# Performance work log

Measured on AMD Instinct MI355X. Metric: run time of the kernel, lower is better.

Reference implementation:

```python
import jax, jax.numpy as jnp
import numpy as np
from jax import lax

H = 64  # LSTM units (hard-coded in the module)


def _lstm(x, W, U, b, return_sequences):
    """Keras-style LSTM (inference; recurrent_dropout inactive).
    x: [B, T, F]; W: [F, 4H]; U: [H, 4H]; b: [4H].
    Gate order (Keras): i, f, g(cell), o.
    """
    B = x.shape[0]
    # Precompute input contribution for all timesteps: [T, B, 4H]
    xz = jnp.einsum('btf,fg->tbg', x, W) + b

    def step(carry, z_t):
        h, c = carry
        z = z_t + h @ U  # [B, 4H]
        i = jax.nn.sigmoid(z[:, :H])
        f = jax.nn.sigmoid(z[:, H:2 * H])
        g = jnp.tanh(z[:, 2 * H:3 * H])
        o = jax.nn.sigmoid(z[:, 3 * H:])
        c = f * c + i * g
        h = o * jnp.tanh(c)
        return (h, c), h

    init = (jnp.zeros((B, H), x.dtype), jnp.zeros((B, H), x.dtype))
    (h_last, _), hs = lax.scan(step, init, xz)
    if return_sequences:
        return jnp.transpose(hs, (1, 0, 2))  # [B, T, H]
    return h_last  # [B, H]


def setup_inputs() -> dict:
    key = jax.random.key(0)
    ks = jax.random.split(key, 8)
    B, T, F = 4096, 256, 32
    s_in = 1.0 / np.sqrt(F)
    s_h = 1.0 / np.sqrt(H)
    return {
        'x': jax.random.normal(ks[0], (B, T, F), jnp.float32),
        'W1': jax.random.normal(ks[1], (F, 4 * H), jnp.float32) * s_in,
        'U1': jax.random.normal(ks[2], (H, 4 * H), jnp.float32) * s_h,
        'b1': jnp.zeros((4 * H,), jnp.float32),
        'W2': jax.random.normal(ks[3], (H, 4 * H), jnp.float32) * s_h,
        'U2': jax.random.normal(ks[4], (H, 4 * H), jnp.float32) * s_h,
        'b2': jnp.zeros((4 * H,), jnp.float32),
        'Wd': jax.random.normal(ks[5], (H, H), jnp.float32) * s_h,
        'bd': jnp.zeros((H,), jnp.float32),
        'Wo': jax.random.normal(ks[6], (H, 1), jnp.float32) * s_h,
        'bo': jnp.zeros((1,), jnp.float32),
    }


def reference(x, W1, U1, b1, W2, U2, b2, Wd, bd, Wo, bo):
    h_seq = _lstm(x, W1, U1, b1, return_sequences=True)   # hidden_lstm
    h_last = _lstm(h_seq, W2, U2, b2, return_sequences=False)  # lstm_layer
    d = jax.nn.sigmoid(h_last @ Wd + bd)  # Dense(64, sigmoid)
    return jax.nn.sigmoid(d @ Wo + bo)    # Dense(1, sigmoid) -> [B, 1]
```

## Files before the change

kernel.cpp:

```cpp
#include <hip/hip_runtime.h>


typedef __attribute__((ext_vector_type(8))) short short8;
typedef __attribute__((ext_vector_type(4))) float floatx4;
typedef __attribute__((ext_vector_type(2))) float floatx2;

__device__ __forceinline__ float ex2(float x){ return __builtin_amdgcn_exp2f(x); }
__device__ __forceinline__ float rcp_(float x){ return __builtin_amdgcn_rcpf(x); }
__device__ __forceinline__ float sigm(float x){ return rcp_(1.0f + ex2(-1.44269504f*x)); }
__device__ __forceinline__ unsigned bfbits(float f){
    unsigned u = __builtin_bit_cast(unsigned, f);
    u += 0x7FFFu + ((u >> 16) & 1u);
    return u >> 16;
}
__device__ __forceinline__ short f2bf(float f){ return (short)bfbits(f); }
__device__ __forceinline__ unsigned pack_bf2(float a, float b){
    return bfbits(a) | (bfbits(b) << 16);
}

#define MFMA_BF16 __builtin_amdgcn_mfma_f32_16x16x32_bf16

__global__ __launch_bounds__(1024, 1)
void lstm2_tz(const float* __restrict__ x,
              const float* __restrict__ W1, const float* __restrict__ U1, const float* __restrict__ b1,
              const float* __restrict__ W2, const float* __restrict__ U2, const float* __restrict__ b2,
              const float* __restrict__ Wd, const float* __restrict__ bd,
              const float* __restrict__ Wo, const float* __restrict__ bo,
              float* __restrict__ out)
{
    __shared__ __align__(16) short h1b[2][16 * 72];
    __shared__ __align__(16) short h2b[2][16 * 72];
    __shared__ __align__(16) short xsb[2][16 * 40];
    __shared__ float psum[4][16];

    const int tid  = threadIdx.x;
    const int w    = tid >> 6;
    const bool isL1 = (w < 8);
    const int wv   = isL1 ? w : (w - 8);
    const int lane = tid & 63;
    const int n    = lane & 15;
    const int q    = lane >> 4;
    const int b0   = blockIdx.x * 16;

    const float LG = 1.44269504f;

    const int ugl = n >> 2;
    const int gA  = n & 3;
    const float sA = (gA == 2) ? (2.0f * LG) : (-LG);

    short8  Wa[8];
    floatx4 bC[2];
    if (isL1) {
#pragma unroll
        for (int tt = 0; tt < 2; ++tt) {
            const int t = wv * 2 + tt;
            const int ncol = gA * 64 + t * 4 + ugl;
#pragma unroll
            for (int j = 0; j < 8; ++j) {
                const int k = q * 8 + j;
                Wa[tt * 3 + 0][j] = f2bf(W1[k * 256 + ncol] * sA);
                Wa[tt * 3 + 1][j] = f2bf(U1[k * 256 + ncol] * sA);
                Wa[tt * 3 + 2][j] = f2bf(U1[(32 + k) * 256 + ncol] * sA);
            }
#pragma unroll
            for (int r = 0; r < 4; ++r)
                bC[tt][r] = b1[r * 64 + t * 4 + q] * ((r == 2) ? (2.0f * LG) : (-LG));
        }
    } else {
#pragma unroll
        for (int tt = 0; tt < 2; ++tt) {
            const int t = wv * 2 + tt;
            const int ncol = gA * 64 + t * 4 + ugl;
#pragma unroll
            for (int j = 0; j < 8; ++j) {
                const int k = q * 8 + j;
                Wa[tt * 4 + 0][j] = f2bf(W2[k * 256 + ncol] * sA);
                Wa[tt * 4 + 1][j] = f2bf(W2[(32 + k) * 256 + ncol] * sA);
                Wa[tt * 4 + 2][j] = f2bf(U2[k * 256 + ncol] * sA);
                Wa[tt * 4 + 3][j] = f2bf(U2[(32 + k) * 256 + ncol] * sA);
            }
#pragma unroll
            for (int r = 0; r < 4; ++r)
                bC[tt][r] = b2[r * 64 + t * 4 + q] * ((r == 2) ? (2.0f * LG) : (-LG));
        }
    }

    {
        unsigned* p1 = (unsigned*)&h1b[0][0];
        unsigned* p2 = (unsigned*)&h2b[0][0];
        for (int i = tid; i < 1152; i += 1024) { p1[i] = 0u; p2[i] = 0u; }
    }

    const int xr = tid >> 4;
    const int xc = (tid & 15) * 2;
    const float* xrow = x + (size_t)(b0 + xr) * 8192 + xc;
    floatx2 xv0;
    if (tid < 256) {
        floatx2 v = *(const floatx2*)xrow;
        *(unsigned*)&xsb[0][xr * 40 + xc] = pack_bf2(v.x, v.y);
        xv0 = *(const floatx2*)(xrow + 32);
    }
    __syncthreads();

    float c[2] = {0, 0};

    for (int u = 0; u <= 256; ++u) {
        const int par = u & 1, pax = par ^ 1;
        if (isL1) {
            if (u < 256) {
                short8 bx  = *(const short8*)&xsb[par][n * 40 + q * 8];
                short8 bh0 = *(const short8*)&h1b[pax][n * 72 + q * 8];
                short8 bh1 = *(const short8*)&h1b[pax][n * 72 + 32 + q * 8];
#pragma unroll
                for (int tt = 0; tt < 2; ++tt) {
                    floatx4 z = bC[tt];
                    z = MFMA_BF16(Wa[tt * 3 + 0], bx,  z, 0, 0, 0);
                    z = MFMA_BF16(Wa[tt * 3 + 1], bh0, z, 0, 0, 0);
                    z = MFMA_BF16(Wa[tt * 3 + 2], bh1, z, 0, 0, 0);
                    float iv = rcp_(1.0f + ex2(z[0]));
                    float fv = rcp_(1.0f + ex2(z[1]));
                    float rg = rcp_(1.0f + ex2(z[2]));
                    float ov = rcp_(1.0f + ex2(z[3]));
                    float gp = fmaf(-5.77078016f, rg, 2.88539008f);
                    c[tt] = fmaf(fv, c[tt], iv * gp);
                    float th = fmaf(-2.0f, rcp_(1.0f + ex2(c[tt])), 1.0f);
                    h1b[par][n * 72 + (wv * 2 + tt) * 4 + q] = f2bf(ov * th);
                }
                if (tid < 256 && u < 255) {
                    *(unsigned*)&xsb[pax][xr * 40 + xc] = pack_bf2(xv0.x, xv0.y);
                    if (u < 254) xv0 = *(const floatx2*)(xrow + (size_t)(u + 2) * 32);
                }
            }
        } else {
            if (u >= 1) {
                short8 bh0 = *(const short8*)&h1b[pax][n * 72 + q * 8];
                short8 bh1 = *(const short8*)&h1b[pax][n * 72 + 32 + q * 8];
                short8 bg0 = *(const short8*)&h2b[par][n * 72 + q * 8];
                short8 bg1 = *(const short8*)&h2b[par][n * 72 + 32 + q * 8];
#pragma unroll
                for (int tt = 0; tt < 2; ++tt) {
                    floatx4 z = bC[tt];
                    z = MFMA_BF16(Wa[tt * 4 + 0], bh0, z, 0, 0, 0);
                    z = MFMA_BF16(Wa[tt * 4 + 1], bh1, z, 0, 0, 0);
                    z = MFMA_BF16(Wa[tt * 4 + 2], bg0, z, 0, 0, 0);
                    z = MFMA_BF16(Wa[tt * 4 + 3], bg1, z, 0, 0, 0);
                    float iv = rcp_(1.0f + ex2(z[0]));
                    float fv = rcp_(1.0f + ex2(z[1]));
                    float rg = rcp_(1.0f + ex2(z[2]));
                    float ov = rcp_(1.0f + ex2(z[3]));
                    float gp = fmaf(-5.77078016f, rg, 2.88539008f);
                    c[tt] = fmaf(fv, c[tt], iv * gp);
                    float th = fmaf(-2.0f, rcp_(1.0f + ex2(c[tt])), 1.0f);
                    h2b[pax][n * 72 + (wv * 2 + tt) * 4 + q] = f2bf(ov * th);
                }
            }
        }
        __syncthreads();
    }

    if (!isL1 && wv < 4) {
        const int colD = wv * 16 + n;
        short8 wd0, wd1;
#pragma unroll
        for (int j = 0; j < 8; ++j) {
            wd0[j] = f2bf(Wd[(q * 8 + j) * 64 + colD] * (-LG));
            wd1[j] = f2bf(Wd[(32 + q * 8 + j) * 64 + colD] * (-LG));
        }
        short8 hA0 = *(const short8*)&h2b[1][n * 72 + q * 8];
        short8 hA1 = *(const short8*)&h2b[1][n * 72 + 32 + q * 8];
        const float bdv = bd[colD] * (-LG);
        floatx4 dacc = { bdv, bdv, bdv, bdv };
        dacc = MFMA_BF16(hA0, wd0, dacc, 0, 0, 0);
        dacc = MFMA_BF16(hA1, wd1, dacc, 0, 0, 0);
        const float wo = Wo[colD];
#pragma unroll
        for (int r = 0; r < 4; ++r) {
            float p = rcp_(1.0f + ex2(dacc[r])) * wo;
            p += __shfl_xor(p, 1, 64);
            p += __shfl_xor(p, 2, 64);
            p += __shfl_xor(p, 4, 64);
            p += __shfl_xor(p, 8, 64);
            if (n == 0) psum[wv][q * 4 + r] = p;
        }
    }
    __syncthreads();
    if (tid < 16) {
        float s = psum[0][tid] + psum[1][tid] + psum[2][tid] + psum[3][tid] + bo[0];
        out[b0 + tid] = sigm(s);
    }
}

extern "C" void kernel_launch(void* const* d_in, const int* in_sizes, int n_in,
                              void* d_out, int out_size, void* d_ws, size_t ws_size,
                              hipStream_t stream) {
    (void)in_sizes; (void)n_in; (void)d_ws; (void)ws_size; (void)out_size;
    const float* x  = (const float*)d_in[0];
    const float* W1 = (const float*)d_in[1];
    const float* U1 = (const float*)d_in[2];
    const float* b1 = (const float*)d_in[3];
    const float* W2 = (const float*)d_in[4];
    const float* U2 = (const float*)d_in[5];
    const float* b2 = (const float*)d_in[6];
    const float* Wd = (const float*)d_in[7];
    const float* bd = (const float*)d_in[8];
    const float* Wo = (const float*)d_in[9];
    const float* bo = (const float*)d_in[10];
    lstm2_tz<<<dim3(256), dim3(1024), 0, stream>>>(
        x, W1, U1, b1, W2, U2, b2, Wd, bd, Wo, bo, (float*)d_out);
}
```

Baseline: 344.0 us.

## Halve block size with four hidden units per lane and XOR-swizzled shared state

Each block now runs 8 waves (4 per LSTM layer) instead of 16. Each lane handles four hidden units instead of two, which doubles the register-held weight fragments. The hidden-state buffers drop their padding and use an XOR swizzle, so each lane writes its four bf16 outputs as one packed 8-byte store using the hardware v_cvt_pk_bf16_f32 conversion. The aim is fewer waves synchronising per timestep, fewer LDS stores, and two blocks resident per CU, at the cost of higher register pressure and more serial MFMA/transcendental work per wave.

```diff
diff --git a/kernel.cpp b/kernel.cpp
--- a/kernel.cpp
+++ b/kernel.cpp
@@ -14,13 +14,15 @@
     return u >> 16;
 }
 __device__ __forceinline__ short f2bf(float f){ return (short)bfbits(f); }
-__device__ __forceinline__ unsigned pack_bf2(float a, float b){
-    return bfbits(a) | (bfbits(b) << 16);
+__device__ __forceinline__ unsigned cvtpk(float lo, float hi){
+    unsigned r;
+    asm("v_cvt_pk_bf16_f32 %0, %1, %2" : "=v"(r) : "v"(lo), "v"(hi));
+    return r;
 }
 
 #define MFMA_BF16 __builtin_amdgcn_mfma_f32_16x16x32_bf16
 
-__global__ __launch_bounds__(1024, 1)
+__global__ __launch_bounds__(512, 2)
 void lstm2_tz(const float* __restrict__ x,
               const float* __restrict__ W1, const float* __restrict__ U1, const float* __restrict__ b1,
               const float* __restrict__ W2, const float* __restrict__ U2, const float* __restrict__ b2,
@@ -28,15 +30,15 @@
               const float* __restrict__ Wo, const float* __restrict__ bo,
               float* __restrict__ out)
 {
-    __shared__ __align__(16) short h1b[2][16 * 72];
-    __shared__ __align__(16) short h2b[2][16 * 72];
+    __shared__ __align__(16) short h1b[2][16 * 64];
+    __shared__ __align__(16) short h2b[2][16 * 64];
     __shared__ __align__(16) short xsb[2][16 * 40];
     __shared__ float psum[4][16];
 
     const int tid  = threadIdx.x;
     const int w    = tid >> 6;
-    const bool isL1 = (w < 8);
-    const int wv   = isL1 ? w : (w - 8);
+    const bool isL1 = (w < 4);
+    const int wv   = isL1 ? w : (w - 4);
     const int lane = tid & 63;
     const int n    = lane & 15;
     const int q    = lane >> 4;
@@ -48,13 +50,19 @@
     const int gA  = n & 3;
     const float sA = (gA == 2) ? (2.0f * LG) : (-LG);
 
-    short8  Wa[8];
-    floatx4 bC[2];
+    const int sw   = n & 7;
+    const int hro0 = n * 64 + ((q ^ sw) << 3);
+    const int hro1 = n * 64 + (((4 + q) ^ sw) << 3);
+    const int xro  = n * 40 + q * 8;
+    const int hwo  = n * 64 + (((wv * 2 + (q >> 1)) ^ sw) << 3) + (q & 1) * 4;
+
+    short8  Wa[16];
+    floatx4 bC[4];
     if (isL1) {
 #pragma unroll
-        for (int tt = 0; tt < 2; ++tt) {
-            const int t = wv * 2 + tt;
-            const int ncol = gA * 64 + t * 4 + ugl;
+        for (int tt = 0; tt < 4; ++tt) {
+            const int un   = wv * 16 + ugl * 4 + tt;
+            const int ncol = gA * 64 + un;
 #pragma unroll
             for (int j = 0; j < 8; ++j) {
                 const int k = q * 8 + j;
@@ -64,13 +72,13 @@
             }
 #pragma unroll
             for (int r = 0; r < 4; ++r)
-                bC[tt][r] = b1[r * 64 + t * 4 + q] * ((r == 2) ? (2.0f * LG) : (-LG));
+                bC[tt][r] = b1[r * 64 + wv * 16 + q * 4 + tt] * ((r == 2) ? (2.0f * LG) : (-LG));
         }
     } else {
 #pragma unroll
-        for (int tt = 0; tt < 2; ++tt) {
-            const int t = wv * 2 + tt;
-            const int ncol = gA * 64 + t * 4 + ugl;
+        for (int tt = 0; tt < 4; ++tt) {
+            const int un   = wv * 16 + ugl * 4 + tt;
+            const int ncol = gA * 64 + un;
 #pragma unroll
             for (int j = 0; j < 8; ++j) {
                 const int k = q * 8 + j;
@@ -81,14 +89,14 @@
             }
 #pragma unroll
             for (int r = 0; r < 4; ++r)
-                bC[tt][r] = b2[r * 64 + t * 4 + q] * ((r == 2) ? (2.0f * LG) : (-LG));
+                bC[tt][r] = b2[r * 64 + wv * 16 + q * 4 + tt] * ((r == 2) ? (2.0f * LG) : (-LG));
         }
     }
 
     {
         unsigned* p1 = (unsigned*)&h1b[0][0];
         unsigned* p2 = (unsigned*)&h2b[0][0];
-        for (int i = tid; i < 1152; i += 1024) { p1[i] = 0u; p2[i] = 0u; }
+        for (int i = tid; i < 1024; i += 512) { p1[i] = 0u; p2[i] = 0u; }
     }
 
     const int xr = tid >> 4;
@@ -97,22 +105,28 @@
     floatx2 xv0;
     if (tid < 256) {
         floatx2 v = *(const floatx2*)xrow;
-        *(unsigned*)&xsb[0][xr * 40 + xc] = pack_bf2(v.x, v.y);
+        *(unsigned*)&xsb[0][xr * 40 + xc] = cvtpk(v.x, v.y);
         xv0 = *(const floatx2*)(xrow + 32);
     }
     __syncthreads();
 
-    float c[2] = {0, 0};
+    float c[4] = {0, 0, 0, 0};
 
     for (int u = 0; u <= 256; ++u) {
         const int par = u & 1, pax = par ^ 1;
         if (isL1) {
             if (u < 256) {
-                short8 bx  = *(const short8*)&xsb[par][n * 40 + q * 8];
-                short8 bh0 = *(const short8*)&h1b[pax][n * 72 + q * 8];
-                short8 bh1 = *(const short8*)&h1b[pax][n * 72 + 32 + q * 8];
-#pragma unroll
-                for (int tt = 0; tt < 2; ++tt) {
+                const short* hR = &h1b[pax][0];
+                short8 bx  = *(const short8*)&xsb[par][xro];
+                short8 bh0 = *(const short8*)&hR[hro0];
+                short8 bh1 = *(const short8*)&hR[hro1];
+                if (tid < 256 && u < 255) {
+                    *(unsigned*)&xsb[pax][xr * 40 + xc] = cvtpk(xv0.x, xv0.y);
+                    if (u < 254) xv0 = *(const floatx2*)(xrow + (size_t)(u + 2) * 32);
+                }
+                float hv[4];
+#pragma unroll
+                for (int tt = 0; tt < 4; ++tt) {
                     floatx4 z = bC[tt];
                     z = MFMA_BF16(Wa[tt * 3 + 0], bx,  z, 0, 0, 0);
                     z = MFMA_BF16(Wa[tt * 3 + 1], bh0, z, 0, 0, 0);
@@ -124,21 +138,22 @@
                     float gp = fmaf(-5.77078016f, rg, 2.88539008f);
                     c[tt] = fmaf(fv, c[tt], iv * gp);
                     float th = fmaf(-2.0f, rcp_(1.0f + ex2(c[tt])), 1.0f);
-                    h1b[par][n * 72 + (wv * 2 + tt) * 4 + q] = f2bf(ov * th);
+                    hv[tt] = ov * th;
                 }
-                if (tid < 256 && u < 255) {
-                    *(unsigned*)&xsb[pax][xr * 40 + xc] = pack_bf2(xv0.x, xv0.y);
-                    if (u < 254) xv0 = *(const floatx2*)(xrow + (size_t)(u + 2) * 32);
-                }
+                uint2 hp; hp.x = cvtpk(hv[0], hv[1]); hp.y = cvtpk(hv[2], hv[3]);
+                *(uint2*)&h1b[par][hwo] = hp;
             }
         } else {
             if (u >= 1) {
-                short8 bh0 = *(const short8*)&h1b[pax][n * 72 + q * 8];
-                short8 bh1 = *(const short8*)&h1b[pax][n * 72 + 32 + q * 8];
-                short8 bg0 = *(const short8*)&h2b[par][n * 72 + q * 8];
-                short8 bg1 = *(const short8*)&h2b[par][n * 72 + 32 + q * 8];
-#pragma unroll
-                for (int tt = 0; tt < 2; ++tt) {
+                const short* hR = &h1b[pax][0];
+                const short* gR = &h2b[par][0];
+                short8 bh0 = *(const short8*)&hR[hro0];
+                short8 bh1 = *(const short8*)&hR[hro1];
+                short8 bg0 = *(const short8*)&gR[hro0];
+                short8 bg1 = *(const short8*)&gR[hro1];
+                float hv[4];
+#pragma unroll
+                for (int tt = 0; tt < 4; ++tt) {
                     floatx4 z = bC[tt];
                     z = MFMA_BF16(Wa[tt * 4 + 0], bh0, z, 0, 0, 0);
                     z = MFMA_BF16(Wa[tt * 4 + 1], bh1, z, 0, 0, 0);
@@ -151,14 +166,16 @@
                     float gp = fmaf(-5.77078016f, rg, 2.88539008f);
                     c[tt] = fmaf(fv, c[tt], iv * gp);
                     float th = fmaf(-2.0f, rcp_(1.0f + ex2(c[tt])), 1.0f);
-                    h2b[pax][n * 72 + (wv * 2 + tt) * 4 + q] = f2bf(ov * th);
+                    hv[tt] = ov * th;
                 }
+                uint2 hp; hp.x = cvtpk(hv[0], hv[1]); hp.y = cvtpk(hv[2], hv[3]);
+                *(uint2*)&h2b[pax][hwo] = hp;
             }
         }
         __syncthreads();
     }
 
-    if (!isL1 && wv < 4) {
+    if (!isL1) {
         const int colD = wv * 16 + n;
         short8 wd0, wd1;
 #pragma unroll
@@ -166,8 +183,8 @@
             wd0[j] = f2bf(Wd[(q * 8 + j) * 64 + colD] * (-LG));
             wd1[j] = f2bf(Wd[(32 + q * 8 + j) * 64 + colD] * (-LG));
         }
-        short8 hA0 = *(const short8*)&h2b[1][n * 72 + q * 8];
-        short8 hA1 = *(const short8*)&h2b[1][n * 72 + 32 + q * 8];
+        short8 hA0 = *(const short8*)&h2b[1][hro0];
+        short8 hA1 = *(const short8*)&h2b[1][hro1];
         const float bdv = bd[colD] * (-LG);
         floatx4 dacc = { bdv, bdv, bdv, bdv };
         dacc = MFMA_BF16(hA0, wd0, dacc, 0, 0, 0);
@@ -205,6 +222,6 @@
     const float* bd = (const float*)d_in[8];
     const float* Wo = (const float*)d_in[9];
     const float* bo = (const float*)d_in[10];
-    lstm2_tz<<<dim3(256), dim3(1024), 0, stream>>>(
+    lstm2_tz<<<dim3(256), dim3(512), 0, stream>>>(
         x, W1, U1, b1, W2, U2, b2, Wd, bd, Wo, bo, (float*)d_out);
 }
```

Result: slower. 354.4 us (+3.0%).
